# Performance work log

Measured on AMD Instinct MI355X. Metric: run time of the kernel, lower is better.

## Reference

```python
import jax, jax.numpy as jnp
import numpy as np

N = 50000
E = 800000
IN_FEATS = 256
NUM_HEADS = 4
OUT_FEATS = 64
NUM_ETYPES = 8
ALPHA = 100.0
NEG_SLOPE_ATTN = 0.2   # self.leaky_relu
NEG_SLOPE_EW = 0.01    # nn.LeakyReLU() default, applied to edge weights


def leaky_relu(x, slope):
    return jnp.where(x >= 0, x, slope * x)


def setup_inputs() -> dict:
    key = jax.random.key(0)
    ks = jax.random.split(key, 8)
    feat = jax.random.normal(ks[0], (N, IN_FEATS), dtype=jnp.float32)
    src = jax.random.randint(ks[1], (E,), 0, N, dtype=jnp.int32)
    dst = jax.random.randint(ks[2], (E,), 0, N, dtype=jnp.int32)
    # etypes are 1-indexed in the original code (edge_weight[edge_feats - 1])
    edge_feats = jax.random.randint(ks[3], (E,), 1, NUM_ETYPES + 1, dtype=jnp.int32)
    # parameters (xavier-normal-ish init for weights; edge_weight = 1/alpha)
    fc_w = jax.random.normal(ks[4], (NUM_HEADS * OUT_FEATS, IN_FEATS), dtype=jnp.float32) * 0.05
    attn_l = jax.random.normal(ks[5], (1, NUM_HEADS, OUT_FEATS), dtype=jnp.float32) * 0.1
    attn_r = jax.random.normal(ks[6], (1, NUM_HEADS, OUT_FEATS), dtype=jnp.float32) * 0.1
    edge_weight = jnp.full((NUM_ETYPES, NUM_HEADS), 1.0 / ALPHA, dtype=jnp.float32)
    return {"feat": feat, "src": src, "dst": dst, "edge_feats": edge_feats,
            "fc_w": fc_w, "attn_l": attn_l, "attn_r": attn_r, "edge_weight": edge_weight}


def reference(feat, src, dst, edge_feats, fc_w, attn_l, attn_r, edge_weight):
    # feat: [N, F_in] -> ft: [N, H, D]
    ft = (feat @ fc_w.T).reshape(-1, NUM_HEADS, OUT_FEATS)
    el = jnp.einsum('nhd,ohd->nh', ft, attn_l)  # [N, H]
    er = jnp.einsum('nhd,ohd->nh', ft, attn_r)  # [N, H]
    # edge-type weights (1-indexed), scaled & leaky-relu'd
    ew = leaky_relu(edge_weight * ALPHA, NEG_SLOPE_EW)  # [T, H]
    ee = ew[edge_feats - 1]                              # [E, H]
    # per-edge logits: u_add_v, times edge weight, leaky relu
    e = leaky_relu((el[src] + er[dst]) * ee, NEG_SLOPE_ATTN)  # [E, H]
    # edge softmax grouped by destination node
    emax = jax.ops.segment_max(e, dst, num_segments=N)        # [N, H]
    ex = jnp.exp(e - emax[dst])
    denom = jax.ops.segment_sum(ex, dst, num_segments=N)      # [N, H]
    a = ex / denom[dst]                                        # [E, H]
    # weighted scatter-sum: sum over edges of a * ft[src]
    msg = ft[src] * a[:, :, None]                              # [E, H, D]
    rst = jax.ops.segment_sum(msg, dst, num_segments=N)       # [N, H, D]
    return rst
```

## Files before the change

### kernel.cpp

```cpp
#include <hip/hip_runtime.h>
#include <hip/hip_bf16.h>


#define NF 256
#define HD 256
#define NH 4
#define PB 256

typedef __attribute__((ext_vector_type(8))) short short8;
typedef __attribute__((ext_vector_type(4))) float f32x4;

static __device__ __forceinline__ unsigned short f2bf(float f) {
  unsigned int u = __float_as_uint(f);
  u += 0x7FFFu + ((u >> 16) & 1u);
  return (unsigned short)(u >> 16);
}
static __device__ __forceinline__ float bf2f(unsigned short s) {
  return __uint_as_float(((unsigned int)s) << 16);
}
static __device__ __forceinline__ unsigned pkbf(float a, float b) {
  __hip_bfloat162 h = __float22bfloat162_rn(make_float2(a, b));
  return *(unsigned*)&h;
}
static __device__ __forceinline__ float wcalc(float sum, float ew) {
  float x = sum * ew;
  x = (x >= 0.f) ? x : 0.2f * x;
  return __expf(x);
}
static __device__ __forceinline__ short8 cvt8(float4 x, float4 y) {
  union { short8 s; uint4 u; } cv;
  cv.u = make_uint4(pkbf(x.x, x.y), pkbf(x.z, x.w),
                    pkbf(y.x, y.y), pkbf(y.z, y.w));
  return cv.s;
}

static __device__ __forceinline__ void gemm_tile(
    const float* __restrict__ feat, const float* __restrict__ fc_w,
    const float* __restrict__ attn_l, const float* __restrict__ attn_r,
    unsigned short* __restrict__ ftb, float* __restrict__ el,
    float* __restrict__ er, int n, int row0, int tid,
    short* aF, short* bF) {
  int lane = tid & 63, w = tid >> 6;

  f32x4 acc[4][4];
#pragma unroll
  for (int i = 0; i < 4; ++i)
#pragma unroll
    for (int j = 0; j < 4; ++j) acc[i][j] = (f32x4){0.f, 0.f, 0.f, 0.f};

  int ar = tid >> 2, ak = (tid & 3) << 4;
  int arow = row0 + ar; if (arow >= n) arow = n - 1;
  const float* ap = feat + (size_t)arow * NF + ak;
  int am = ar & 15, art = ar >> 4;
  int s0 = ak >> 5, q0 = (ak >> 3) & 3;
  int s1 = (ak + 8) >> 5, q1 = ((ak + 8) >> 3) & 3;
  short* aw0 = &aF[(((art * 2 + s0) * 64) + q0 * 16 + am) * 8];
  short* aw1 = &aF[(((art * 2 + s1) * 64) + q1 * 16 + am) * 8];

  const float* bp = fc_w + (size_t)tid * NF;
  int bn = tid & 15, bcg = tid >> 4;

  for (int k0 = 0; k0 < NF; k0 += 64) {
    float4 f0 = *(const float4*)(ap + k0);
    float4 f1 = *(const float4*)(ap + k0 + 4);
    float4 f2 = *(const float4*)(ap + k0 + 8);
    float4 f3 = *(const float4*)(ap + k0 + 12);
    uint4 oa = make_uint4(pkbf(f0.x, f0.y), pkbf(f0.z, f0.w),
                          pkbf(f1.x, f1.y), pkbf(f1.z, f1.w));
    uint4 ob = make_uint4(pkbf(f2.x, f2.y), pkbf(f2.z, f2.w),
                          pkbf(f3.x, f3.y), pkbf(f3.z, f3.w));
    *(uint4*)aw0 = oa;
    *(uint4*)aw1 = ob;
#pragma unroll
    for (int o8 = 0; o8 < 8; ++o8) {
      float4 bx = *(const float4*)(bp + k0 + o8 * 8);
      float4 by = *(const float4*)(bp + k0 + o8 * 8 + 4);
      short8 bv = cvt8(bx, by);
      int bs = o8 >> 2, bq = o8 & 3;
      *(short8*)&bF[(((bcg * 2 + bs) * 64) + bq * 16 + bn) * 8] = bv;
    }
    __syncthreads();
#pragma unroll
    for (int s = 0; s < 2; ++s) {
      short8 af[4], bfr[4];
#pragma unroll
      for (int rt = 0; rt < 4; ++rt)
        af[rt] = *(const short8*)&aF[(((rt * 2 + s) * 64) + lane) * 8];
#pragma unroll
      for (int ct = 0; ct < 4; ++ct)
        bfr[ct] = *(const short8*)&bF[((((w * 4 + ct) * 2 + s) * 64) + lane) * 8];
#pragma unroll
      for (int rt = 0; rt < 4; ++rt)
#pragma unroll
        for (int ct = 0; ct < 4; ++ct)
          acc[rt][ct] = __builtin_amdgcn_mfma_f32_16x16x32_bf16(
              af[rt], bfr[ct], acc[rt][ct], 0, 0, 0);
    }
    __syncthreads();
  }

  int ln = lane & 15, lq = lane >> 4;
  float al4[4], ar4[4];
#pragma unroll
  for (int ct = 0; ct < 4; ++ct) {
    al4[ct] = attn_l[w * 64 + ct * 16 + ln];
    ar4[ct] = attn_r[w * 64 + ct * 16 + ln];
  }
#pragma unroll
  for (int rt = 0; rt < 4; ++rt) {
#pragma unroll
    for (int r = 0; r < 4; ++r) {
      float pl = 0.f, pr = 0.f;
#pragma unroll
      for (int ct = 0; ct < 4; ++ct) {
        float v = acc[rt][ct][r];
        pl += v * al4[ct]; pr += v * ar4[ct];
      }
#pragma unroll
      for (int off = 1; off <= 8; off <<= 1) {
        pl += __shfl_xor(pl, off);
        pr += __shfl_xor(pr, off);
      }
      int row = row0 + rt * 16 + lq * 4 + r;
      if (row < n) {
        if (ln == 0) { el[row * NH + w] = pl; er[row * NH + w] = pr; }
        unsigned short* fr = ftb + (size_t)row * HD + w * 64 + ln;
#pragma unroll
        for (int ct = 0; ct < 4; ++ct) fr[ct * 16] = f2bf(acc[rt][ct][r]);
      }
    }
  }
}

__global__ __launch_bounds__(256) void hist_gemm_k(
    const int* __restrict__ dst, int* __restrict__ ghist, int e, int epb, int hb,
    const float* __restrict__ feat, const float* __restrict__ fc_w,
    const float* __restrict__ attn_l, const float* __restrict__ attn_r,
    unsigned short* __restrict__ ftb, float* __restrict__ el,
    float* __restrict__ er, int n) {
  __shared__ short aF[4 * 2 * 64 * 8];
  __shared__ short bF[16 * 2 * 64 * 8];
  int tid = threadIdx.x;
  if (blockIdx.x < hb) {
    int* bins = (int*)aF;
    int blk = blockIdx.x;
    bins[tid] = 0;
    __syncthreads();
    int e0 = blk * epb, e1 = e0 + epb; if (e1 > e) e1 = e;
    for (int i = e0 + tid; i < e1; i += 256)
      atomicAdd(&bins[dst[i] >> 8], 1);
    __syncthreads();
    ghist[blk * 256 + tid] = bins[tid];
    return;
  }
  gemm_tile(feat, fc_w, attn_l, attn_r, ftb, el, er, n,
            ((int)blockIdx.x - hb) * 64, tid, aF, bF);
}

__global__ __launch_bounds__(256) void scan_k(
    const int* __restrict__ ghist, int* __restrict__ lsg,
    int* __restrict__ bb, int nblk) {
  int tid = threadIdx.x;
  int run = 0;
  int i = 0;
  for (; i + 8 <= nblk; i += 8) {
    int v[8];
#pragma unroll
    for (int j = 0; j < 8; ++j) v[j] = ghist[(i + j) * 256 + tid];
#pragma unroll
    for (int j = 0; j < 8; ++j) { lsg[(i + j) * 256 + tid] = run; run += v[j]; }
  }
  for (; i < nblk; ++i) {
    int v = ghist[i * 256 + tid];
    lsg[i * 256 + tid] = run;
    run += v;
  }
  __shared__ int wt[4];
  int lane = tid & 63, wid = tid >> 6;
  int inc = run;
#pragma unroll
  for (int off = 1; off < 64; off <<= 1) {
    int t = __shfl_up(inc, off);
    if (lane >= off) inc += t;
  }
  if (lane == 63) wt[wid] = inc;
  __syncthreads();
  int base = 0;
  if (wid > 0) base += wt[0];
  if (wid > 1) base += wt[1];
  if (wid > 2) base += wt[2];
  bb[tid] = base + inc - run;
  if (tid == 255) bb[256] = base + inc;
}

__global__ __launch_bounds__(256) void scat_gemm_k(
    const int* __restrict__ src, const int* __restrict__ dst,
    const int* __restrict__ efeats, const int* __restrict__ lsg,
    const int* __restrict__ bb, int* __restrict__ mid, int e, int epb, int sb,
    const float* __restrict__ feat, const float* __restrict__ fc_w,
    const float* __restrict__ attn_l, const float* __restrict__ attn_r,
    unsigned short* __restrict__ ftb, float* __restrict__ el,
    float* __restrict__ er, int n, int tile0) {
  __shared__ short aF[4 * 2 * 64 * 8];
  __shared__ short bF[16 * 2 * 64 * 8];
  int tid = threadIdx.x;
  if (blockIdx.x < sb) {
    int* cur = (int*)aF;
    int blk = blockIdx.x;
    cur[tid] = bb[tid] + lsg[blk * 256 + tid];
    __syncthreads();
    int e0 = blk * epb, e1 = e0 + epb; if (e1 > e) e1 = e;
    for (int i = e0 + tid; i < e1; i += 256) {
      int d = dst[i];
      int pos = atomicAdd(&cur[d >> 8], 1);
      mid[pos] = src[i] | ((efeats[i] - 1) << 17) | ((d & 255) << 20);
    }
    return;
  }
  gemm_tile(feat, fc_w, attn_l, attn_r, ftb, el, er, n,
            (tile0 + (int)blockIdx.x - sb) * 64, tid, aF, bF);
}

__global__ __launch_bounds__(256) void bucket_k(
    const int* __restrict__ mid, const int* __restrict__ bb,
    int* __restrict__ poffs, int* __restrict__ pk, int nN) {
  __shared__ int cnt[256];
  __shared__ int cur[256];
  int tid = threadIdx.x, b = blockIdx.x;
  int bb0 = bb[b];
  int bb1 = bb[b + 1];
  cnt[tid] = 0;
  __syncthreads();
  for (int i = bb0 + tid; i < bb1; i += 256)
    atomicAdd(&cnt[(mid[i] >> 20) & 255], 1);
  __syncthreads();
  if (tid < 64) {
    int carry = 0;
#pragma unroll
    for (int c = 0; c < 4; ++c) {
      int v = cnt[c * 64 + tid];
      int inc = v;
#pragma unroll
      for (int off = 1; off < 64; off <<= 1) {
        int t2 = __shfl_up(inc, off);
        if (tid >= off) inc += t2;
      }
      cur[c * 64 + tid] = inc - v + carry;
      carry += __shfl(inc, 63);
    }
  }
  __syncthreads();
  int node = b * 256 + tid;
  int g = bb0 + cur[tid];
  if (node <= nN) poffs[node] = g;
  cur[tid] = g;
  __syncthreads();
  for (int i = bb0 + tid; i < bb1; i += 256) {
    int v = mid[i];
    int pos = atomicAdd(&cur[(v >> 20) & 255], 1);
    pk[pos] = v & 0xFFFFF;
  }
}

__global__ __launch_bounds__(256) void agg3_k(
    const unsigned short* __restrict__ ftb, const int* __restrict__ pk,
    const float* __restrict__ el, const float* __restrict__ er,
    const float* __restrict__ ewt, const int* __restrict__ offs,
    float* __restrict__ out, int n) {
  __shared__ float ew_s[32];
  if (threadIdx.x < 32) {
    float v = ewt[threadIdx.x] * 100.0f;
    ew_s[threadIdx.x] = (v >= 0.f) ? v : 0.01f * v;
  }
  __syncthreads();
  int node = blockIdx.x * 4 + (threadIdx.x >> 6);
  int lane = threadIdx.x & 63;
  if (node >= n) return;
  int start = offs[node];
  int deg = offs[node + 1] - start;
  float o0 = 0.f, o1 = 0.f, o2 = 0.f, o3 = 0.f;
  if (deg > 0) {
    int hl = lane >> 4;
    float er_h = er[(size_t)node * NH + hl];
    const unsigned short* fb = ftb + (size_t)lane * 4;
    const float* elh = el + hl;
    const int* pg = pk + start;
    float ss = 0.f;
    int i = 0;
    for (; i + 8 <= deg; i += 8) {
      int4 pa = *(const int4*)(pg + i);
      int4 pb = *(const int4*)(pg + i + 4);
      int sA = pa.x & 0x1FFFF, tA = pa.x >> 17;
      int sB = pa.y & 0x1FFFF, tB = pa.y >> 17;
      int sC = pa.z & 0x1FFFF, tC = pa.z >> 17;
      int sD = pa.w & 0x1FFFF, tD = pa.w >> 17;
      int sE = pb.x & 0x1FFFF, tE = pb.x >> 17;
      int sF = pb.y & 0x1FFFF, tF = pb.y >> 17;
      int sG = pb.z & 0x1FFFF, tG = pb.z >> 17;
      int sH = pb.w & 0x1FFFF, tH = pb.w >> 17;
      float eA = elh[sA * NH], eB = elh[sB * NH], eC = elh[sC * NH], eD = elh[sD * NH];
      float eE = elh[sE * NH], eF = elh[sF * NH], eG = elh[sG * NH], eH = elh[sH * NH];
      ushort4 fA = *(const ushort4*)(fb + (size_t)sA * HD);
      ushort4 fB = *(const ushort4*)(fb + (size_t)sB * HD);
      ushort4 fC = *(const ushort4*)(fb + (size_t)sC * HD);
      ushort4 fD = *(const ushort4*)(fb + (size_t)sD * HD);
      ushort4 fE = *(const ushort4*)(fb + (size_t)sE * HD);
      ushort4 fF = *(const ushort4*)(fb + (size_t)sF * HD);
      ushort4 fG = *(const ushort4*)(fb + (size_t)sG * HD);
      ushort4 fH = *(const ushort4*)(fb + (size_t)sH * HD);
      float wA = wcalc(eA + er_h, ew_s[tA * NH + hl]);
      float wB = wcalc(eB + er_h, ew_s[tB * NH + hl]);
      float wC = wcalc(eC + er_h, ew_s[tC * NH + hl]);
      float wD = wcalc(eD + er_h, ew_s[tD * NH + hl]);
      float wE = wcalc(eE + er_h, ew_s[tE * NH + hl]);
      float wF = wcalc(eF + er_h, ew_s[tF * NH + hl]);
      float wG = wcalc(eG + er_h, ew_s[tG * NH + hl]);
      float wH = wcalc(eH + er_h, ew_s[tH * NH + hl]);
      ss += ((wA + wB) + (wC + wD)) + ((wE + wF) + (wG + wH));
      o0 = fmaf(wA, bf2f(fA.x), o0); o1 = fmaf(wA, bf2f(fA.y), o1);
      o2 = fmaf(wA, bf2f(fA.z), o2); o3 = fmaf(wA, bf2f(fA.w), o3);
      o0 = fmaf(wB, bf2f(fB.x), o0); o1 = fmaf(wB, bf2f(fB.y), o1);
      o2 = fmaf(wB, bf2f(fB.z), o2); o3 = fmaf(wB, bf2f(fB.w), o3);
      o0 = fmaf(wC, bf2f(fC.x), o0); o1 = fmaf(wC, bf2f(fC.y), o1);
      o2 = fmaf(wC, bf2f(fC.z), o2); o3 = fmaf(wC, bf2f(fC.w), o3);
      o0 = fmaf(wD, bf2f(fD.x), o0); o1 = fmaf(wD, bf2f(fD.y), o1);
      o2 = fmaf(wD, bf2f(fD.z), o2); o3 = fmaf(wD, bf2f(fD.w), o3);
      o0 = fmaf(wE, bf2f(fE.x), o0); o1 = fmaf(wE, bf2f(fE.y), o1);
      o2 = fmaf(wE, bf2f(fE.z), o2); o3 = fmaf(wE, bf2f(fE.w), o3);
      o0 = fmaf(wF, bf2f(fF.x), o0); o1 = fmaf(wF, bf2f(fF.y), o1);
      o2 = fmaf(wF, bf2f(fF.z), o2); o3 = fmaf(wF, bf2f(fF.w), o3);
      o0 = fmaf(wG, bf2f(fG.x), o0); o1 = fmaf(wG, bf2f(fG.y), o1);
      o2 = fmaf(wG, bf2f(fG.z), o2); o3 = fmaf(wG, bf2f(fG.w), o3);
      o0 = fmaf(wH, bf2f(fH.x), o0); o1 = fmaf(wH, bf2f(fH.y), o1);
      o2 = fmaf(wH, bf2f(fH.z), o2); o3 = fmaf(wH, bf2f(fH.w), o3);
    }
    for (; i < deg; ++i) {
      int pv = pg[i];
      int sA = pv & 0x1FFFF, tA = pv >> 17;
      float eA = elh[sA * NH];
      ushort4 fA = *(const ushort4*)(fb + (size_t)sA * HD);
      float wA = wcalc(eA + er_h, ew_s[tA * NH + hl]);
      ss += wA;
      o0 = fmaf(wA, bf2f(fA.x), o0); o1 = fmaf(wA, bf2f(fA.y), o1);
      o2 = fmaf(wA, bf2f(fA.z), o2); o3 = fmaf(wA, bf2f(fA.w), o3);
    }
    float rs = 1.0f / ss;
    o0 *= rs; o1 *= rs; o2 *= rs; o3 *= rs;
  }
  *(float4*)(out + (size_t)node * HD + lane * 4) = make_float4(o0, o1, o2, o3);
}

extern "C" void kernel_launch(void* const* d_in, const int* in_sizes, int n_in,
                              void* d_out, int out_size, void* d_ws, size_t ws_size,
                              hipStream_t stream) {
  const float* feat   = (const float*)d_in[0];
  const int*   src    = (const int*)d_in[1];
  const int*   dst    = (const int*)d_in[2];
  const int*   efeats = (const int*)d_in[3];
  const float* fc_w   = (const float*)d_in[4];
  const float* attn_l = (const float*)d_in[5];
  const float* attn_r = (const float*)d_in[6];
  const float* ewt    = (const float*)d_in[7];
  float* out = (float*)d_out;

  int N = in_sizes[0] / NF;
  int E = in_sizes[1];

  char* ws = (char*)d_ws;
  size_t off = 0;
  unsigned short* ftb = (unsigned short*)(ws + off); off += (size_t)N * HD * 2;
  float* el  = (float*)(ws + off);  off += (size_t)N * NH * 4;
  float* er  = (float*)(ws + off);  off += (size_t)N * NH * 4;
  int* poffs = (int*)(ws + off);    off += ((size_t)N + 16) * 4;
  int* ghist = (int*)(ws + off);    off += (size_t)PB * 256 * 4;
  int* lsg   = (int*)(ws + off);    off += (size_t)PB * 256 * 4;
  int* bb    = (int*)(ws + off);    off += 260 * 4;
  int* mid   = (int*)(ws + off);    off += (size_t)E * 4;
  int* pk    = (int*)(ws + off);    off += (size_t)E * 4;

  int gb = (N + 63) / 64;
  int g1 = 430;
  int g2 = gb - g1;
  int epb = (E + PB - 1) / PB;
  int nbuck = (N + 255) >> 8;

  hist_gemm_k<<<PB + g1, 256, 0, stream>>>(dst, ghist, E, epb, PB,
                                           feat, fc_w, attn_l, attn_r,
                                           ftb, el, er, N);
  scan_k<<<1, 256, 0, stream>>>(ghist, lsg, bb, PB);
  scat_gemm_k<<<PB + g2, 256, 0, stream>>>(src, dst, efeats, lsg, bb, mid,
                                           E, epb, PB,
                                           feat, fc_w, attn_l, attn_r,
                                           ftb, el, er, N, g1);
  bucket_k<<<nbuck, 256, 0, stream>>>(mid, bb, poffs, pk, N);
  agg3_k<<<(N + 3) / 4, 256, 0, stream>>>(ftb, pk, el, er, ewt, poffs, out, N);
}
```

Baseline: 249.9 us.

## Load weight fragments directly from global and double-buffer the A tile in LDS

The GEMM tile no longer stages fc_w through shared memory. Each lane now loads its B fragment directly from global memory and converts it to bf16 in registers. The A tile in LDS is double-buffered, so the next K-slice is written while the current one is consumed, which removes one barrier per iteration and cuts the LDS footprint. The cost is more global loads of fc_w per block, relying on the cache since every block rereads the same weights, plus the extra register pressure of the in-register conversion.

```diff
diff --git a/kernel.cpp b/kernel.cpp
--- a/kernel.cpp
+++ b/kernel.cpp
@@ -38,9 +38,9 @@
     const float* __restrict__ feat, const float* __restrict__ fc_w,
     const float* __restrict__ attn_l, const float* __restrict__ attn_r,
     unsigned short* __restrict__ ftb, float* __restrict__ el,
-    float* __restrict__ er, int n, int row0, int tid,
-    short* aF, short* bF) {
+    float* __restrict__ er, int n, int row0, int tid, short* aF) {
   int lane = tid & 63, w = tid >> 6;
+  int rr = lane & 15, kq = lane >> 4;
 
   f32x4 acc[4][4];
 #pragma unroll
@@ -54,41 +54,55 @@
   int am = ar & 15, art = ar >> 4;
   int s0 = ak >> 5, q0 = (ak >> 3) & 3;
   int s1 = (ak + 8) >> 5, q1 = ((ak + 8) >> 3) & 3;
-  short* aw0 = &aF[(((art * 2 + s0) * 64) + q0 * 16 + am) * 8];
-  short* aw1 = &aF[(((art * 2 + s1) * 64) + q1 * 16 + am) * 8];
-
-  const float* bp = fc_w + (size_t)tid * NF;
-  int bn = tid & 15, bcg = tid >> 4;
-
-  for (int k0 = 0; k0 < NF; k0 += 64) {
-    float4 f0 = *(const float4*)(ap + k0);
-    float4 f1 = *(const float4*)(ap + k0 + 4);
-    float4 f2 = *(const float4*)(ap + k0 + 8);
-    float4 f3 = *(const float4*)(ap + k0 + 12);
+  int aw0o = (((art * 2 + s0) * 64) + q0 * 16 + am) * 8;
+  int aw1o = (((art * 2 + s1) * 64) + q1 * 16 + am) * 8;
+
+  const float* bp[4];
+#pragma unroll
+  for (int ct = 0; ct < 4; ++ct)
+    bp[ct] = fc_w + (size_t)(w * 64 + ct * 16 + rr) * NF + kq * 8;
+
+  {
+    float4 f0 = *(const float4*)(ap);
+    float4 f1 = *(const float4*)(ap + 4);
+    float4 f2 = *(const float4*)(ap + 8);
+    float4 f3 = *(const float4*)(ap + 12);
     uint4 oa = make_uint4(pkbf(f0.x, f0.y), pkbf(f0.z, f0.w),
                           pkbf(f1.x, f1.y), pkbf(f1.z, f1.w));
     uint4 ob = make_uint4(pkbf(f2.x, f2.y), pkbf(f2.z, f2.w),
                           pkbf(f3.x, f3.y), pkbf(f3.z, f3.w));
-    *(uint4*)aw0 = oa;
-    *(uint4*)aw1 = ob;
-#pragma unroll
-    for (int o8 = 0; o8 < 8; ++o8) {
-      float4 bx = *(const float4*)(bp + k0 + o8 * 8);
-      float4 by = *(const float4*)(bp + k0 + o8 * 8 + 4);
-      short8 bv = cvt8(bx, by);
-      int bs = o8 >> 2, bq = o8 & 3;
-      *(short8*)&bF[(((bcg * 2 + bs) * 64) + bq * 16 + bn) * 8] = bv;
-    }
+    *(uint4*)&aF[aw0o] = oa;
+    *(uint4*)&aF[aw1o] = ob;
+  }
+
+  int buf = 0;
+  for (int k0 = 0; k0 < NF; k0 += 64) {
     __syncthreads();
+    if (k0 + 64 < NF) {
+      float4 f0 = *(const float4*)(ap + k0 + 64);
+      float4 f1 = *(const float4*)(ap + k0 + 68);
+      float4 f2 = *(const float4*)(ap + k0 + 72);
+      float4 f3 = *(const float4*)(ap + k0 + 76);
+      uint4 oa = make_uint4(pkbf(f0.x, f0.y), pkbf(f0.z, f0.w),
+                            pkbf(f1.x, f1.y), pkbf(f1.z, f1.w));
+      uint4 ob = make_uint4(pkbf(f2.x, f2.y), pkbf(f2.z, f2.w),
+                            pkbf(f3.x, f3.y), pkbf(f3.z, f3.w));
+      int bo = (buf ^ 1) * 4096;
+      *(uint4*)&aF[bo + aw0o] = oa;
+      *(uint4*)&aF[bo + aw1o] = ob;
+    }
 #pragma unroll
     for (int s = 0; s < 2; ++s) {
       short8 af[4], bfr[4];
 #pragma unroll
       for (int rt = 0; rt < 4; ++rt)
-        af[rt] = *(const short8*)&aF[(((rt * 2 + s) * 64) + lane) * 8];
-#pragma unroll
-      for (int ct = 0; ct < 4; ++ct)
-        bfr[ct] = *(const short8*)&bF[((((w * 4 + ct) * 2 + s) * 64) + lane) * 8];
+        af[rt] = *(const short8*)&aF[buf * 4096 + (((rt * 2 + s) * 64) + lane) * 8];
+#pragma unroll
+      for (int ct = 0; ct < 4; ++ct) {
+        float4 bx = *(const float4*)(bp[ct] + k0 + s * 32);
+        float4 by = *(const float4*)(bp[ct] + k0 + s * 32 + 4);
+        bfr[ct] = cvt8(bx, by);
+      }
 #pragma unroll
       for (int rt = 0; rt < 4; ++rt)
 #pragma unroll
@@ -96,7 +110,7 @@
           acc[rt][ct] = __builtin_amdgcn_mfma_f32_16x16x32_bf16(
               af[rt], bfr[ct], acc[rt][ct], 0, 0, 0);
     }
-    __syncthreads();
+    buf ^= 1;
   }
 
   int ln = lane & 15, lq = lane >> 4;
@@ -138,8 +152,7 @@
     const float* __restrict__ attn_l, const float* __restrict__ attn_r,
     unsigned short* __restrict__ ftb, float* __restrict__ el,
     float* __restrict__ er, int n) {
-  __shared__ short aF[4 * 2 * 64 * 8];
-  __shared__ short bF[16 * 2 * 64 * 8];
+  __shared__ short aF[2 * 4 * 2 * 64 * 8];
   int tid = threadIdx.x;
   if (blockIdx.x < hb) {
     int* bins = (int*)aF;
@@ -154,7 +167,7 @@
     return;
   }
   gemm_tile(feat, fc_w, attn_l, attn_r, ftb, el, er, n,
-            ((int)blockIdx.x - hb) * 64, tid, aF, bF);
+            ((int)blockIdx.x - hb) * 64, tid, aF);
 }
 
 __global__ __launch_bounds__(256) void scan_k(
@@ -201,8 +214,7 @@
     const float* __restrict__ attn_l, const float* __restrict__ attn_r,
     unsigned short* __restrict__ ftb, float* __restrict__ el,
     float* __restrict__ er, int n, int tile0) {
-  __shared__ short aF[4 * 2 * 64 * 8];
-  __shared__ short bF[16 * 2 * 64 * 8];
+  __shared__ short aF[2 * 4 * 2 * 64 * 8];
   int tid = threadIdx.x;
   if (blockIdx.x < sb) {
     int* cur = (int*)aF;
@@ -218,7 +230,7 @@
     return;
   }
   gemm_tile(feat, fc_w, attn_l, attn_r, ftb, el, er, n,
-            (tile0 + (int)blockIdx.x - sb) * 64, tid, aF, bF);
+            (tile0 + (int)blockIdx.x - sb) * 64, tid, aF);
 }
 
 __global__ __launch_bounds__(256) void bucket_k(
```

After: 249.7 us. No clear change (-0.1%).
